# Performance work log

Measured on AMD Instinct MI355X. Metric: run time of the kernel, lower is better.

## Reference

```python
import jax, jax.numpy as jnp
import numpy as np

S = 1024          # tokens (prefill)
DIM = 2560
HEAD_DIM = 128
N_HEADS = 20
N_KV = 5
HPG = N_HEADS // N_KV      # heads per kv group = 4
GS = 128                   # weight-scale group size
THETA = 500000.0
EPS = 1e-05
QKV_OUT = (N_HEADS + 2 * N_KV) * HEAD_DIM  # 3840


def setup_inputs() -> dict:
    key = jax.random.key(0)
    ks = jax.random.split(key, 7)
    x = jax.random.normal(ks[0], (S, DIM), jnp.float32)
    # unpacked int2 (ternary) weights, stored as float for the reference math
    w_qkv = jax.random.randint(ks[1], (QKV_OUT, DIM), -1, 2).astype(jnp.float32)
    ws_qkv = jax.random.uniform(ks[2], (QKV_OUT, DIM // GS), jnp.float32, 0.01, 0.05)
    w_o = jax.random.randint(ks[3], (DIM, N_HEADS * HEAD_DIM), -1, 2).astype(jnp.float32)
    ws_o = jax.random.uniform(ks[4], (DIM, N_HEADS * HEAD_DIM // GS), jnp.float32, 0.01, 0.05)
    q_norm_w = 1.0 + 0.02 * jax.random.normal(ks[5], (HEAD_DIM,), jnp.float32)
    k_norm_w = 1.0 + 0.02 * jax.random.normal(ks[6], (HEAD_DIM,), jnp.float32)
    return {"x": x, "w_qkv": w_qkv, "ws_qkv": ws_qkv, "w_o": w_o, "ws_o": ws_o,
            "q_norm_w": q_norm_w, "k_norm_w": k_norm_w}


def _quant_act(x):
    # per-token symmetric int8 quant: s = 127 / max|x| (clamped)
    s = 127.0 / jnp.clip(jnp.max(jnp.abs(x), axis=-1, keepdims=True), 1e-05, None)
    q = jnp.clip(jnp.round(x * s), -128.0, 127.0)
    return q, s


def _bitlinear(x, w, ws):
    # int8 activation x int2 weight GEMM with per-(out,group) dequant scales
    q, s = _quant_act(x)
    w_dq = w * jnp.repeat(ws, GS, axis=1)        # [out, in]
    return (q @ w_dq.T) / s


def _rmsnorm(x, w):
    return x * jax.lax.rsqrt(jnp.mean(x * x, axis=-1, keepdims=True) + EPS) * w


def _rope(x, cos, sin):
    # x: [S, ..., d]; cos/sin: [S, d//2], interleaved-pair (llama) convention
    d2 = x.shape[-1] // 2
    shape = (x.shape[0],) + (1,) * (x.ndim - 2) + (d2,)
    c = cos.reshape(shape)
    s = sin.reshape(shape)
    xr = x.reshape(x.shape[:-1] + (d2, 2))
    x0, x1 = xr[..., 0], xr[..., 1]
    out = jnp.stack([x0 * c - x1 * s, x0 * s + x1 * c], axis=-1)
    return out.reshape(x.shape)


def reference(x, w_qkv, ws_qkv, w_o, ws_o, q_norm_w, k_norm_w):
    qkv = _bitlinear(x, w_qkv, ws_qkv)                       # [S, 3840]
    q_size = N_HEADS * HEAD_DIM
    k_size = N_KV * HEAD_DIM
    xq = qkv[:, :q_size].reshape(S, N_KV, HPG, HEAD_DIM)     # [S, g, h, d]
    xk = qkv[:, q_size:q_size + k_size].reshape(S, N_KV, HEAD_DIM)
    xv = qkv[:, q_size + k_size:].reshape(S, N_KV, HEAD_DIM)
    xq = _rmsnorm(xq, q_norm_w)
    xk = _rmsnorm(xk, k_norm_w)
    # RoPE (prefill: positions 0..S-1)
    pos = jnp.arange(S, dtype=jnp.float32)
    inv_freq = THETA ** (-jnp.arange(0, HEAD_DIM, 2, dtype=jnp.float32) / HEAD_DIM)
    ang = pos[:, None] * inv_freq[None, :]                   # [S, d/2]
    cos, sin = jnp.cos(ang), jnp.sin(ang)
    xq = _rope(xq, cos, sin)
    xk = _rope(xk, cos, sin)
    # GQA causal flash-attention math
    scale = HEAD_DIM ** -0.5
    scores = jnp.einsum('sghd,tgd->ghst', xq, xk) * scale    # [g, h, S, S]
    causal = jnp.tril(jnp.ones((S, S), bool))
    scores = jnp.where(causal, scores, -1e30)
    attn = jax.nn.softmax(scores, axis=-1)
    out = jnp.einsum('ghst,tgd->sghd', attn, xv).reshape(S, N_HEADS * HEAD_DIM)
    return _bitlinear(out, w_o, ws_o)                        # [S, DIM]
```

## Files before the change

kernel.cpp:

```cpp
#include <hip/hip_runtime.h>
#include <hip/hip_bf16.h>
#include <cstdint>
#include <math.h>

#define SEQ 1024
#define DIM 2560
#define HD 128
#define NH 20
#define NKV 5
#define QKV_OUT 3840
#define GS 128

typedef __bf16 bf16;
typedef __bf16 bf16x4 __attribute__((ext_vector_type(4)));
typedef __bf16 bf16x8 __attribute__((ext_vector_type(8)));
typedef float f32x4 __attribute__((ext_vector_type(4)));

__global__ __launch_bounds__(256) void quant_kernel(
    const float* __restrict__ x, bf16* __restrict__ act,
    float* __restrict__ rs, int cols) {
  const int row = blockIdx.x;
  const int tid = threadIdx.x;
  const float* xr = x + (size_t)row * cols;
  float m = 0.f;
  for (int i = tid; i < cols; i += 256) m = fmaxf(m, fabsf(xr[i]));
  for (int off = 32; off; off >>= 1) m = fmaxf(m, __shfl_xor(m, off));
  __shared__ float red[4];
  __shared__ float s_bc;
  if ((tid & 63) == 0) red[tid >> 6] = m;
  __syncthreads();
  if (tid == 0) {
    float mm = fmaxf(fmaxf(red[0], red[1]), fmaxf(red[2], red[3]));
    mm = fmaxf(mm, 1e-5f);
    s_bc = 127.f / mm;
    rs[row] = mm / 127.f;
  }
  __syncthreads();
  const float s = s_bc;
  bf16* ar = act + (size_t)row * cols;
  for (int i = tid; i < cols; i += 256) {
    float q = rintf(xr[i] * s);
    q = fminf(fmaxf(q, -128.f), 127.f);
    ar[i] = (bf16)q;
  }
}

__global__ __launch_bounds__(256) void dequant_kernel(
    const float* __restrict__ w, const float* __restrict__ ws,
    bf16* __restrict__ wdq, int K, long total4) {
  long i = (long)blockIdx.x * 256 + threadIdx.x;
  if (i >= total4) return;
  long e = i * 4;
  int row = (int)(e / K);
  int k = (int)(e % K);
  float sc = ws[(size_t)row * (K / GS) + (k / GS)];
  float4 wv = *(const float4*)(w + e);
  bf16x4 o;
  o[0] = (bf16)(wv.x * sc);
  o[1] = (bf16)(wv.y * sc);
  o[2] = (bf16)(wv.z * sc);
  o[3] = (bf16)(wv.w * sc);
  *(bf16x4*)(wdq + e) = o;
}

__device__ __forceinline__ void gload_lds16(const bf16* g, bf16* l) {
  __builtin_amdgcn_global_load_lds(
      (const __attribute__((address_space(1))) void*)g,
      (__attribute__((address_space(3))) void*)l, 16, 0, 0);
}

__global__ __launch_bounds__(256) void gemm_bt(
    const bf16* __restrict__ A, const bf16* __restrict__ B,
    const float* __restrict__ rs, float* __restrict__ C,
    int N, int K, int Kh, size_t part_stride) {
  __shared__ bf16 As[64 * 64];
  __shared__ bf16 Bs[128 * 64];
  const int tid = threadIdx.x;
  const int w = tid >> 6, l = tid & 63;
  const int row0 = blockIdx.y * 64;
  const int col0 = blockIdx.x * 128;
  const int z = blockIdx.z;
  const int wm = (w >> 1) * 32, wn = (w & 1) * 64;
  const int lcol = l & 15, quad = l >> 4;
  const int sr = l >> 3;
  const int sg = l & 7;
  const bf16* Ag = A + (size_t)row0 * K + (size_t)z * Kh;
  const bf16* Bg = B + (size_t)col0 * K + (size_t)z * Kh;

  f32x4 acc[2][4] = {};

  for (int k0 = 0; k0 < Kh; k0 += 64) {
    __syncthreads();
#pragma unroll
    for (int i = 0; i < 2; ++i) {
      int rb = w * 16 + i * 8;
      int r = rb + sr;
      gload_lds16(Ag + (size_t)r * K + k0 + ((sg ^ (r & 7)) * 8), As + rb * 64);
    }
#pragma unroll
    for (int i = 0; i < 4; ++i) {
      int rb = w * 32 + i * 8;
      int r = rb + sr;
      gload_lds16(Bg + (size_t)r * K + k0 + ((sg ^ (r & 7)) * 8), Bs + rb * 64);
    }
    __syncthreads();
#pragma unroll
    for (int ks = 0; ks < 2; ++ks) {
      bf16x8 af[2], bff[4];
#pragma unroll
      for (int mi = 0; mi < 2; ++mi) {
        int R = wm + mi * 16 + lcol;
        af[mi] = *(const bf16x8*)(As + R * 64 + (((ks * 4 + quad) ^ (R & 7)) * 8));
      }
#pragma unroll
      for (int ni = 0; ni < 4; ++ni) {
        int R = wn + ni * 16 + lcol;
        bff[ni] = *(const bf16x8*)(Bs + R * 64 + (((ks * 4 + quad) ^ (R & 7)) * 8));
      }
#pragma unroll
      for (int mi = 0; mi < 2; ++mi)
#pragma unroll
        for (int ni = 0; ni < 4; ++ni)
          acc[mi][ni] = __builtin_amdgcn_mfma_f32_16x16x32_bf16(
              af[mi], bff[ni], acc[mi][ni], 0, 0, 0);
    }
  }
  float* Cp = C + (size_t)z * part_stride;
#pragma unroll
  for (int mi = 0; mi < 2; ++mi) {
#pragma unroll
    for (int ni = 0; ni < 4; ++ni) {
      int col = col0 + wn + ni * 16 + lcol;
#pragma unroll
      for (int r = 0; r < 4; ++r) {
        int row = row0 + wm + mi * 16 + quad * 4 + r;
        Cp[(size_t)row * N + col] = acc[mi][ni][r] * rs[row];
      }
    }
  }
}

__global__ __launch_bounds__(256) void add2_kernel(
    const float* __restrict__ a, const float* __restrict__ b,
    float* __restrict__ o, int n4) {
  int i = blockIdx.x * 256 + threadIdx.x;
  if (i >= n4) return;
  float4 x = ((const float4*)a)[i];
  float4 y = ((const float4*)b)[i];
  ((float4*)o)[i] = make_float4(x.x + y.x, x.y + y.y, x.z + y.z, x.w + y.w);
}

__global__ void qk_post(const float* __restrict__ qkvA, const float* __restrict__ qkvB,
                        const float* __restrict__ qw, const float* __restrict__ kw,
                        bf16* __restrict__ Qo, bf16* __restrict__ Ko) {
  const int t = blockIdx.x, h = blockIdx.y, i = threadIdx.x;
  const size_t off = (h < NH)
      ? (size_t)t * QKV_OUT + h * HD
      : (size_t)t * QKV_OUT + 2560 + (h - NH) * HD;
  const float* s1 = qkvA + off;
  const float* s2 = qkvB + off;
  float x0 = s1[2 * i] + s2[2 * i];
  float x1 = s1[2 * i + 1] + s2[2 * i + 1];
  float ss = x0 * x0 + x1 * x1;
  for (int off2 = 1; off2 < 64; off2 <<= 1) ss += __shfl_xor(ss, off2);
  float r = rsqrtf(ss * (1.f / 128.f) + 1e-5f);
  const float* wv = (h < NH) ? qw : kw;
  float y0 = x0 * r * wv[2 * i];
  float y1 = x1 * r * wv[2 * i + 1];
  float inv_freq = powf(500000.f, -(float)(2 * i) * (1.f / 128.f));
  float ang = (float)t * inv_freq;
  float sn, cs;
  sincosf(ang, &sn, &cs);
  float o0 = y0 * cs - y1 * sn;
  float o1 = y0 * sn + y1 * cs;
  if (h < NH) {
    bf16* dst = Qo + ((size_t)t * NH + h) * HD + 2 * i;
    dst[0] = (bf16)o0; dst[1] = (bf16)o1;
  } else {
    bf16* dst = Ko + ((size_t)(h - NH) * SEQ + t) * HD + 2 * i;
    dst[0] = (bf16)o0; dst[1] = (bf16)o1;
  }
}

__global__ __launch_bounds__(256) void v_post(const float* __restrict__ qkvA,
                                              const float* __restrict__ qkvB,
                                              bf16* __restrict__ Vt) {
  const int t0 = blockIdx.x * 64, g = blockIdx.y;
  const int tid = threadIdx.x;
  __shared__ bf16 Ls[64 * 137];
  {
    const int tl = tid >> 4;
    const int d0 = (tid & 15) * 8;
#pragma unroll
    for (int pass = 0; pass < 4; ++pass) {
      int t = pass * 16 + tl;
      size_t off = (size_t)(t0 + t) * QKV_OUT + 3200 + g * HD + d0;
      float4 a = *(const float4*)(qkvA + off);
      float4 b = *(const float4*)(qkvA + off + 4);
      float4 a2 = *(const float4*)(qkvB + off);
      float4 b2 = *(const float4*)(qkvB + off + 4);
      bf16* dst = Ls + t * 137 + d0;
      dst[0] = (bf16)(a.x + a2.x); dst[1] = (bf16)(a.y + a2.y);
      dst[2] = (bf16)(a.z + a2.z); dst[3] = (bf16)(a.w + a2.w);
      dst[4] = (bf16)(b.x + b2.x); dst[5] = (bf16)(b.y + b2.y);
      dst[6] = (bf16)(b.z + b2.z); dst[7] = (bf16)(b.w + b2.w);
    }
  }
  __syncthreads();
  {
    const int dl = tid >> 3;
    const int tl0 = (tid & 7) * 8;
#pragma unroll
    for (int pass = 0; pass < 4; ++pass) {
      int d = pass * 32 + dl;
      bf16x8 v;
#pragma unroll
      for (int j = 0; j < 8; ++j) v[j] = Ls[(tl0 + j) * 137 + d];
      *(bf16x8*)(Vt + ((size_t)g * HD + d) * SEQ + t0 + tl0) = v;
    }
  }
}

__global__ __launch_bounds__(128) void attn_mfma(
    const bf16* __restrict__ Qb, const bf16* __restrict__ Kb,
    const bf16* __restrict__ Vt, float* __restrict__ O) {
  const int qb = 31 - (int)blockIdx.x;
  const int H = blockIdx.y, g = H >> 2;
  const int tid = threadIdx.x;
  const int wave = tid >> 6, lane = tid & 63;
  const int qcol = lane & 15, quad = lane >> 4;
  const int q_tok = qb * 32 + wave * 16 + qcol;
  const float scale = 0.08838834764831843f;

  __shared__ bf16 Ks[64 * 128];
  __shared__ bf16 Vs[128 * 64];

  const bf16* kbase = Kb + (size_t)g * SEQ * HD;
  const bf16* vbase = Vt + (size_t)g * HD * SEQ;

  bf16x8 qf[4];
  {
    const bf16* qp = Qb + ((size_t)q_tok * NH + H) * HD + quad * 8;
#pragma unroll
    for (int kc = 0; kc < 4; ++kc) qf[kc] = *(const bf16x8*)(qp + kc * 32);
  }

  float m_i = -1e30f, l_i = 0.f;
  f32x4 o_acc[8] = {};
  const int kt_max = (qb * 32 + 31) >> 6;

  const int k_r = lane >> 4, k_g = lane & 15;
  const int v_r = lane >> 3, v_g = lane & 7;

  for (int kt = 0; kt <= kt_max; ++kt) {
    const int key0 = kt * 64;
    __syncthreads();
#pragma unroll
    for (int p = 0; p < 8; ++p) {
      int r0 = (wave * 8 + p) * 4;
      int r = r0 + k_r;
      gload_lds16(kbase + (size_t)(key0 + r) * HD + ((k_g ^ (r & 15)) * 8),
                  Ks + r0 * 128);
    }
#pragma unroll
    for (int p = 0; p < 8; ++p) {
      int r0 = (wave * 8 + p) * 8;
      int r = r0 + v_r;
      gload_lds16(vbase + (size_t)r * SEQ + key0 + ((v_g ^ (r & 7)) * 8),
                  Vs + r0 * 64);
    }
    __syncthreads();

    f32x4 s[4];
#pragma unroll
    for (int mg = 0; mg < 4; ++mg) {
      const int R = mg * 16 + qcol;
      const bf16* krow = Ks + R * 128;
      f32x4 acc = {0.f, 0.f, 0.f, 0.f};
#pragma unroll
      for (int kc = 0; kc < 4; ++kc) {
        int j = kc * 4 + quad;
        bf16x8 kf = *(const bf16x8*)(krow + ((j ^ (R & 15)) * 8));
        acc = __builtin_amdgcn_mfma_f32_16x16x32_bf16(kf, qf[kc], acc, 0, 0, 0);
      }
      s[mg] = acc;
    }

    float mt = -1e30f;
#pragma unroll
    for (int mg = 0; mg < 4; ++mg)
#pragma unroll
      for (int r = 0; r < 4; ++r) {
        int key = key0 + mg * 16 + quad * 4 + r;
        float v = (key <= q_tok) ? s[mg][r] * scale : -1e30f;
        s[mg][r] = v;
        mt = fmaxf(mt, v);
      }
    mt = fmaxf(mt, __shfl_xor(mt, 16));
    mt = fmaxf(mt, __shfl_xor(mt, 32));
    float mnew = fmaxf(m_i, mt);
    float alpha = __expf(m_i - mnew);
    float ps = 0.f;
#pragma unroll
    for (int mg = 0; mg < 4; ++mg)
#pragma unroll
      for (int r = 0; r < 4; ++r) {
        float pv = __expf(s[mg][r] - mnew);
        s[mg][r] = pv;
        ps += pv;
      }
    ps += __shfl_xor(ps, 16);
    ps += __shfl_xor(ps, 32);
    l_i = l_i * alpha + ps;
    m_i = mnew;
#pragma unroll
    for (int mg2 = 0; mg2 < 8; ++mg2)
#pragma unroll
      for (int r = 0; r < 4; ++r) o_acc[mg2][r] *= alpha;

    bf16x8 pb[2];
#pragma unroll
    for (int c = 0; c < 2; ++c)
#pragma unroll
      for (int j = 0; j < 8; ++j)
        pb[c][j] = (bf16)s[c * 2 + (j >> 2)][j & 3];

#pragma unroll
    for (int mg2 = 0; mg2 < 8; ++mg2) {
      const int R = mg2 * 16 + qcol;
      const bf16* vrow = Vs + R * 64;
      f32x4 acc = o_acc[mg2];
#pragma unroll
      for (int c = 0; c < 2; ++c) {
        int g8a = c * 8 + quad;
        int g8b = c * 8 + 4 + quad;
        bf16x4 v0 = *(const bf16x4*)(vrow + ((g8a >> 1) ^ (R & 7)) * 8 + (g8a & 1) * 4);
        bf16x4 v1 = *(const bf16x4*)(vrow + ((g8b >> 1) ^ (R & 7)) * 8 + (g8b & 1) * 4);
        bf16x8 vfr;
#pragma unroll
        for (int j = 0; j < 4; ++j) { vfr[j] = v0[j]; vfr[j + 4] = v1[j]; }
        acc = __builtin_amdgcn_mfma_f32_16x16x32_bf16(vfr, pb[c], acc, 0, 0, 0);
      }
      o_acc[mg2] = acc;
    }
  }

  const float inv = 1.f / l_i;
  float* op = O + (size_t)q_tok * DIM + H * HD + quad * 4;
#pragma unroll
  for (int mg2 = 0; mg2 < 8; ++mg2) {
    float4 vv = make_float4(o_acc[mg2][0] * inv, o_acc[mg2][1] * inv,
                            o_acc[mg2][2] * inv, o_acc[mg2][3] * inv);
    *(float4*)(op + mg2 * 16) = vv;
  }
}

extern "C" void kernel_launch(void* const* d_in, const int* in_sizes, int n_in,
                              void* d_out, int out_size, void* d_ws, size_t ws_size,
                              hipStream_t stream) {
  const float* x      = (const float*)d_in[0];
  const float* w_qkv  = (const float*)d_in[1];
  const float* ws_qkv = (const float*)d_in[2];
  const float* w_o    = (const float*)d_in[3];
  const float* ws_o   = (const float*)d_in[4];
  const float* qnw    = (const float*)d_in[5];
  const float* knw    = (const float*)d_in[6];
  float* out = (float*)d_out;

  char* p = (char*)d_ws;
  bf16*  act1 = (bf16*)p;  p += (size_t)SEQ * DIM * 2;
  float* rs1  = (float*)p; p += 4096;
  bf16*  wqdq = (bf16*)p;  p += (size_t)QKV_OUT * DIM * 2;
  bf16*  wodq = (bf16*)p;  p += (size_t)DIM * DIM * 2;
  float* qkvA = (float*)p; p += (size_t)SEQ * QKV_OUT * 4;
  float* qkvB = (float*)p; p += (size_t)SEQ * QKV_OUT * 4;
  bf16*  Qb   = (bf16*)p;  p += (size_t)SEQ * NH * HD * 2;
  bf16*  Kb   = (bf16*)p;  p += (size_t)NKV * SEQ * HD * 2;
  bf16*  Vt   = (bf16*)p;  p += (size_t)NKV * HD * SEQ * 2;
  float* attn = (float*)p; p += (size_t)SEQ * DIM * 4;
  bf16*  act2 = (bf16*)p;  p += (size_t)SEQ * DIM * 2;
  float* rs2  = (float*)p; p += 4096;

  float* outA = qkvA;
  float* outB = qkvA + (size_t)SEQ * DIM;

  quant_kernel<<<SEQ, 256, 0, stream>>>(x, act1, rs1, DIM);
  {
    long t4 = (long)QKV_OUT * DIM / 4;
    dequant_kernel<<<(int)((t4 + 255) / 256), 256, 0, stream>>>(w_qkv, ws_qkv, wqdq, DIM, t4);
  }
  {
    long t4 = (long)DIM * DIM / 4;
    dequant_kernel<<<(int)((t4 + 255) / 256), 256, 0, stream>>>(w_o, ws_o, wodq, DIM, t4);
  }
  gemm_bt<<<dim3(QKV_OUT / 128, SEQ / 64, 2), 256, 0, stream>>>(
      act1, wqdq, rs1, qkvA, QKV_OUT, DIM, DIM / 2, (size_t)SEQ * QKV_OUT);
  qk_post<<<dim3(SEQ, 25), 64, 0, stream>>>(qkvA, qkvB, qnw, knw, Qb, Kb);
  v_post<<<dim3(SEQ / 64, NKV), 256, 0, stream>>>(qkvA, qkvB, Vt);
  attn_mfma<<<dim3(32, NH), 128, 0, stream>>>(Qb, Kb, Vt, attn);
  quant_kernel<<<SEQ, 256, 0, stream>>>(attn, act2, rs2, DIM);
  gemm_bt<<<dim3(DIM / 128, SEQ / 64, 2), 256, 0, stream>>>(
      act2, wodq, rs2, outA, DIM, DIM, DIM / 2, (size_t)SEQ * DIM);
  {
    int n4 = SEQ * DIM / 4;
    add2_kernel<<<(n4 + 255) / 256, 256, 0, stream>>>(outA, outB, out, n4);
  }
}
```

Before: 246.6 us.

## Double-buffer attention over head pairs, bf16 attn output, drop split-K output GEMM

Attention blocks now run 4 waves covering two heads of the same KV group, so each staged K/V tile is shared. K/V tiles are double-buffered, with the next tile's global-to-LDS load issued before computing on the current one. Attention output is written as bf16 and quantized by a templated quant kernel. The output projection uses a new 64x64 non-split GEMM that writes straight to the result, which removes the partial-sum buffer and the add kernel. The two weight-dequant launches are merged into one. Risks are lower occupancy from the doubled LDS, and extra rounding from the bf16 intermediate before int8 quantization.

After: 242.9 us. About the same (-1.5%).

```diff
diff --git a/kernel.cpp b/kernel.cpp
--- a/kernel.cpp
+++ b/kernel.cpp
@@ -16,14 +16,15 @@
 typedef __bf16 bf16x8 __attribute__((ext_vector_type(8)));
 typedef float f32x4 __attribute__((ext_vector_type(4)));
 
+template <typename T>
 __global__ __launch_bounds__(256) void quant_kernel(
-    const float* __restrict__ x, bf16* __restrict__ act,
+    const T* __restrict__ x, bf16* __restrict__ act,
     float* __restrict__ rs, int cols) {
   const int row = blockIdx.x;
   const int tid = threadIdx.x;
-  const float* xr = x + (size_t)row * cols;
+  const T* xr = x + (size_t)row * cols;
   float m = 0.f;
-  for (int i = tid; i < cols; i += 256) m = fmaxf(m, fabsf(xr[i]));
+  for (int i = tid; i < cols; i += 256) m = fmaxf(m, fabsf((float)xr[i]));
   for (int off = 32; off; off >>= 1) m = fmaxf(m, __shfl_xor(m, off));
   __shared__ float red[4];
   __shared__ float s_bc;
@@ -39,28 +40,31 @@
   const float s = s_bc;
   bf16* ar = act + (size_t)row * cols;
   for (int i = tid; i < cols; i += 256) {
-    float q = rintf(xr[i] * s);
+    float q = rintf((float)xr[i] * s);
     q = fminf(fmaxf(q, -128.f), 127.f);
     ar[i] = (bf16)q;
   }
 }
 
-__global__ __launch_bounds__(256) void dequant_kernel(
-    const float* __restrict__ w, const float* __restrict__ ws,
-    bf16* __restrict__ wdq, int K, long total4) {
+__global__ __launch_bounds__(256) void dequant2_kernel(
+    const float* __restrict__ w1, const float* __restrict__ ws1, bf16* __restrict__ o1,
+    const float* __restrict__ w2, const float* __restrict__ ws2, bf16* __restrict__ o2,
+    long n1_4, long total4) {
   long i = (long)blockIdx.x * 256 + threadIdx.x;
   if (i >= total4) return;
-  long e = i * 4;
-  int row = (int)(e / K);
-  int k = (int)(e % K);
-  float sc = ws[(size_t)row * (K / GS) + (k / GS)];
+  const float* w; const float* ws; bf16* o; long e;
+  if (i < n1_4) { w = w1; ws = ws1; o = o1; e = i * 4; }
+  else          { w = w2; ws = ws2; o = o2; e = (i - n1_4) * 4; }
+  int row = (int)(e / DIM);
+  int k = (int)(e % DIM);
+  float sc = ws[(size_t)row * (DIM / GS) + (k / GS)];
   float4 wv = *(const float4*)(w + e);
-  bf16x4 o;
-  o[0] = (bf16)(wv.x * sc);
-  o[1] = (bf16)(wv.y * sc);
-  o[2] = (bf16)(wv.z * sc);
-  o[3] = (bf16)(wv.w * sc);
-  *(bf16x4*)(wdq + e) = o;
+  bf16x4 ov;
+  ov[0] = (bf16)(wv.x * sc);
+  ov[1] = (bf16)(wv.y * sc);
+  ov[2] = (bf16)(wv.z * sc);
+  ov[3] = (bf16)(wv.w * sc);
+  *(bf16x4*)(o + e) = ov;
 }
 
 __device__ __forceinline__ void gload_lds16(const bf16* g, bf16* l) {
@@ -140,14 +144,72 @@
   }
 }
 
-__global__ __launch_bounds__(256) void add2_kernel(
-    const float* __restrict__ a, const float* __restrict__ b,
-    float* __restrict__ o, int n4) {
-  int i = blockIdx.x * 256 + threadIdx.x;
-  if (i >= n4) return;
-  float4 x = ((const float4*)a)[i];
-  float4 y = ((const float4*)b)[i];
-  ((float4*)o)[i] = make_float4(x.x + y.x, x.y + y.y, x.z + y.z, x.w + y.w);
+__global__ __launch_bounds__(256) void gemm_bt64(
+    const bf16* __restrict__ A, const bf16* __restrict__ B,
+    const float* __restrict__ rs, float* __restrict__ C, int N, int K) {
+  __shared__ bf16 As[64 * 64];
+  __shared__ bf16 Bs[64 * 64];
+  const int tid = threadIdx.x;
+  const int w = tid >> 6, l = tid & 63;
+  const int row0 = blockIdx.y * 64;
+  const int col0 = blockIdx.x * 64;
+  const int wm = (w >> 1) * 32, wn = (w & 1) * 32;
+  const int lcol = l & 15, quad = l >> 4;
+  const int sr = l >> 3;
+  const int sg = l & 7;
+  const bf16* Ag = A + (size_t)row0 * K;
+  const bf16* Bg = B + (size_t)col0 * K;
+
+  f32x4 acc[2][2] = {};
+
+  for (int k0 = 0; k0 < K; k0 += 64) {
+    __syncthreads();
+#pragma unroll
+    for (int i = 0; i < 2; ++i) {
+      int rb = w * 16 + i * 8;
+      int r = rb + sr;
+      gload_lds16(Ag + (size_t)r * K + k0 + ((sg ^ (r & 7)) * 8), As + rb * 64);
+    }
+#pragma unroll
+    for (int i = 0; i < 2; ++i) {
+      int rb = w * 16 + i * 8;
+      int r = rb + sr;
+      gload_lds16(Bg + (size_t)r * K + k0 + ((sg ^ (r & 7)) * 8), Bs + rb * 64);
+    }
+    __syncthreads();
+#pragma unroll
+    for (int ks = 0; ks < 2; ++ks) {
+      bf16x8 af[2], bff[2];
+#pragma unroll
+      for (int mi = 0; mi < 2; ++mi) {
+        int R = wm + mi * 16 + lcol;
+        af[mi] = *(const bf16x8*)(As + R * 64 + (((ks * 4 + quad) ^ (R & 7)) * 8));
+      }
+#pragma unroll
+      for (int ni = 0; ni < 2; ++ni) {
+        int R = wn + ni * 16 + lcol;
+        bff[ni] = *(const bf16x8*)(Bs + R * 64 + (((ks * 4 + quad) ^ (R & 7)) * 8));
+      }
+#pragma unroll
+      for (int mi = 0; mi < 2; ++mi)
+#pragma unroll
+        for (int ni = 0; ni < 2; ++ni)
+          acc[mi][ni] = __builtin_amdgcn_mfma_f32_16x16x32_bf16(
+              af[mi], bff[ni], acc[mi][ni], 0, 0, 0);
+    }
+  }
+#pragma unroll
+  for (int mi = 0; mi < 2; ++mi) {
+#pragma unroll
+    for (int ni = 0; ni < 2; ++ni) {
+      int col = col0 + wn + ni * 16 + lcol;
+#pragma unroll
+      for (int r = 0; r < 4; ++r) {
+        int row = row0 + wm + mi * 16 + quad * 4 + r;
+        C[(size_t)row * N + col] = acc[mi][ni][r] * rs[row];
+      }
+    }
+  }
 }
 
 __global__ void qk_post(const float* __restrict__ qkvA, const float* __restrict__ qkvB,
@@ -221,19 +283,21 @@
   }
 }
 
-__global__ __launch_bounds__(128) void attn_mfma(
+__global__ __launch_bounds__(256) void attn_mfma(
     const bf16* __restrict__ Qb, const bf16* __restrict__ Kb,
-    const bf16* __restrict__ Vt, float* __restrict__ O) {
+    const bf16* __restrict__ Vt, bf16* __restrict__ O) {
   const int qb = 31 - (int)blockIdx.x;
-  const int H = blockIdx.y, g = H >> 2;
+  const int hp = blockIdx.y;
   const int tid = threadIdx.x;
   const int wave = tid >> 6, lane = tid & 63;
+  const int H = (hp >> 1) * 4 + (hp & 1) * 2 + (wave >> 1);
+  const int g = H >> 2;
   const int qcol = lane & 15, quad = lane >> 4;
-  const int q_tok = qb * 32 + wave * 16 + qcol;
+  const int q_tok = qb * 32 + (wave & 1) * 16 + qcol;
   const float scale = 0.08838834764831843f;
 
-  __shared__ bf16 Ks[64 * 128];
-  __shared__ bf16 Vs[128 * 64];
+  __shared__ bf16 Ks[2][64 * 128];
+  __shared__ bf16 Vs[2][128 * 64];
 
   const bf16* kbase = Kb + (size_t)g * SEQ * HD;
   const bf16* vbase = Vt + (size_t)g * HD * SEQ;
@@ -252,30 +316,36 @@
   const int k_r = lane >> 4, k_g = lane & 15;
   const int v_r = lane >> 3, v_g = lane & 7;
 
+#define STAGE(buf, key0)                                                       \
+  {                                                                            \
+    _Pragma("unroll") for (int p = 0; p < 4; ++p) {                            \
+      int r0 = wave * 16 + p * 4;                                              \
+      int r = r0 + k_r;                                                        \
+      gload_lds16(kbase + (size_t)((key0) + r) * HD + ((k_g ^ (r & 15)) * 8),  \
+                  &Ks[buf][r0 * 128]);                                         \
+    }                                                                          \
+    _Pragma("unroll") for (int p = 0; p < 4; ++p) {                            \
+      int r0 = wave * 32 + p * 8;                                              \
+      int r = r0 + v_r;                                                        \
+      gload_lds16(vbase + (size_t)r * SEQ + (key0) + ((v_g ^ (r & 7)) * 8),    \
+                  &Vs[buf][r0 * 64]);                                          \
+    }                                                                          \
+  }
+
+  STAGE(0, 0)
+
   for (int kt = 0; kt <= kt_max; ++kt) {
     const int key0 = kt * 64;
     __syncthreads();
-#pragma unroll
-    for (int p = 0; p < 8; ++p) {
-      int r0 = (wave * 8 + p) * 4;
-      int r = r0 + k_r;
-      gload_lds16(kbase + (size_t)(key0 + r) * HD + ((k_g ^ (r & 15)) * 8),
-                  Ks + r0 * 128);
-    }
-#pragma unroll
-    for (int p = 0; p < 8; ++p) {
-      int r0 = (wave * 8 + p) * 8;
-      int r = r0 + v_r;
-      gload_lds16(vbase + (size_t)r * SEQ + key0 + ((v_g ^ (r & 7)) * 8),
-                  Vs + r0 * 64);
-    }
-    __syncthreads();
+    if (kt < kt_max) STAGE((kt + 1) & 1, key0 + 64)
+    const bf16* Kt = Ks[kt & 1];
+    const bf16* Vtile = Vs[kt & 1];
 
     f32x4 s[4];
 #pragma unroll
     for (int mg = 0; mg < 4; ++mg) {
       const int R = mg * 16 + qcol;
-      const bf16* krow = Ks + R * 128;
+      const bf16* krow = Kt + R * 128;
       f32x4 acc = {0.f, 0.f, 0.f, 0.f};
 #pragma unroll
       for (int kc = 0; kc < 4; ++kc) {
@@ -328,7 +398,7 @@
 #pragma unroll
     for (int mg2 = 0; mg2 < 8; ++mg2) {
       const int R = mg2 * 16 + qcol;
-      const bf16* vrow = Vs + R * 64;
+      const bf16* vrow = Vtile + R * 64;
       f32x4 acc = o_acc[mg2];
 #pragma unroll
       for (int c = 0; c < 2; ++c) {
@@ -344,14 +414,18 @@
       o_acc[mg2] = acc;
     }
   }
+#undef STAGE
 
   const float inv = 1.f / l_i;
-  float* op = O + (size_t)q_tok * DIM + H * HD + quad * 4;
+  bf16* op = O + (size_t)q_tok * DIM + H * HD + quad * 4;
 #pragma unroll
   for (int mg2 = 0; mg2 < 8; ++mg2) {
-    float4 vv = make_float4(o_acc[mg2][0] * inv, o_acc[mg2][1] * inv,
-                            o_acc[mg2][2] * inv, o_acc[mg2][3] * inv);
-    *(float4*)(op + mg2 * 16) = vv;
+    bf16x4 vv;
+    vv[0] = (bf16)(o_acc[mg2][0] * inv);
+    vv[1] = (bf16)(o_acc[mg2][1] * inv);
+    vv[2] = (bf16)(o_acc[mg2][2] * inv);
+    vv[3] = (bf16)(o_acc[mg2][3] * inv);
+    *(bf16x4*)(op + mg2 * 16) = vv;
   }
 }
 
@@ -377,32 +451,23 @@
   bf16*  Qb   = (bf16*)p;  p += (size_t)SEQ * NH * HD * 2;
   bf16*  Kb   = (bf16*)p;  p += (size_t)NKV * SEQ * HD * 2;
   bf16*  Vt   = (bf16*)p;  p += (size_t)NKV * HD * SEQ * 2;
-  float* attn = (float*)p; p += (size_t)SEQ * DIM * 4;
+  bf16*  attn = (bf16*)p;  p += (size_t)SEQ * DIM * 2;
   bf16*  act2 = (bf16*)p;  p += (size_t)SEQ * DIM * 2;
   float* rs2  = (float*)p; p += 4096;
 
-  float* outA = qkvA;
-  float* outB = qkvA + (size_t)SEQ * DIM;
-
-  quant_kernel<<<SEQ, 256, 0, stream>>>(x, act1, rs1, DIM);
+  quant_kernel<float><<<SEQ, 256, 0, stream>>>(x, act1, rs1, DIM);
   {
-    long t4 = (long)QKV_OUT * DIM / 4;
-    dequant_kernel<<<(int)((t4 + 255) / 256), 256, 0, stream>>>(w_qkv, ws_qkv, wqdq, DIM, t4);
-  }
-  {
-    long t4 = (long)DIM * DIM / 4;
-    dequant_kernel<<<(int)((t4 + 255) / 256), 256, 0, stream>>>(w_o, ws_o, wodq, DIM, t4);
+    long n1_4 = (long)QKV_OUT * DIM / 4;
+    long total4 = n1_4 + (long)DIM * DIM / 4;
+    dequant2_kernel<<<(int)((total4 + 255) / 256), 256, 0, stream>>>(
+        w_qkv, ws_qkv, wqdq, w_o, ws_o, wodq, n1_4, total4);
   }
   gemm_bt<<<dim3(QKV_OUT / 128, SEQ / 64, 2), 256, 0, stream>>>(
       act1, wqdq, rs1, qkvA, QKV_OUT, DIM, DIM / 2, (size_t)SEQ * QKV_OUT);
   qk_post<<<dim3(SEQ, 25), 64, 0, stream>>>(qkvA, qkvB, qnw, knw, Qb, Kb);
   v_post<<<dim3(SEQ / 64, NKV), 256, 0, stream>>>(qkvA, qkvB, Vt);
-  attn_mfma<<<dim3(32, NH), 128, 0, stream>>>(Qb, Kb, Vt, attn);
-  quant_kernel<<<SEQ, 256, 0, stream>>>(attn, act2, rs2, DIM);
-  gemm_bt<<<dim3(DIM / 128, SEQ / 64, 2), 256, 0, stream>>>(
-      act2, wodq, rs2, outA, DIM, DIM, DIM / 2, (size_t)SEQ * DIM);
-  {
-    int n4 = SEQ * DIM / 4;
-    add2_kernel<<<(n4 + 255) / 256, 256, 0, stream>>>(outA, outB, out, n4);
-  }
-}
+  attn_mfma<<<dim3(32, 10), 256, 0, stream>>>(Qb, Kb, Vt, attn);
+  quant_kernel<bf16><<<SEQ, 256, 0, stream>>>(attn, act2, rs2, DIM);
+  gemm_bt64<<<dim3(DIM / 64, SEQ / 64), 256, 0, stream>>>(
+      act2, wodq, rs2, out, DIM, DIM);
+}
```
